# Performance work log

Hardware: AMD Instinct MI355X
Metric: run time of the kernel (lower is better)

The kernel has to match this reference:

```python
import jax, jax.numpy as jnp
import numpy as np

B, N, H = 16, 1024, 1024


def setup_inputs() -> dict:
    key = jax.random.key(0)
    ks = jax.random.split(key, 12)
    inv = 1.0 / np.sqrt(H)
    inp = {
        "x": jax.random.normal(ks[0], (B, N, H), jnp.float32),
        "atom_graph": jax.random.normal(ks[1], (B, N, N), jnp.float32),
        "variable_graph": jax.random.normal(ks[2], (B, N, N), jnp.float32),
        "Wq": jax.random.uniform(ks[3], (H, H), jnp.float32, -inv, inv),
        "bq": jax.random.uniform(ks[4], (H,), jnp.float32, -inv, inv),
        "Wk": jax.random.uniform(ks[5], (H, H), jnp.float32, -inv, inv),
        "bk": jax.random.uniform(ks[6], (H,), jnp.float32, -inv, inv),
        "Wv": jax.random.uniform(ks[7], (H, H), jnp.float32, -inv, inv),
        "bv": jax.random.uniform(ks[8], (H,), jnp.float32, -inv, inv),
        "predicate_pos": jax.random.randint(ks[9], (B, N), 0, 2, jnp.int32),
        "variable_tags": jax.random.randint(ks[10], (B, N), 0, 4, jnp.int32),
    }
    return inp


def _path_pool(h, predicate_pos):
    # h: [B,N,H]; predicate_pos: [B,N] in {0,1}
    b, n, d = h.shape
    i = jnp.arange(n)
    # pos[i-2] (value irrelevant for i<2, those branches handled explicitly)
    pp2 = jnp.pad(predicate_pos, ((0, 0), (2, 0)))[:, :n]  # [B,N]
    # window [s, e): i==0 -> [0,2); i==1 -> [0,3); pos[i-2]==1 -> [i,i+2); else [i-1,i+2)
    s = jnp.where(i < 2, 0, jnp.where(pp2 == 1, i, i - 1))  # [B,N]
    e = jnp.where(i == 0, 2, jnp.where(i == 1, 3, i + 2))    # [N]
    e = jnp.minimum(e, n)
    e = jnp.broadcast_to(e, (b, n))
    # prefix sums along node dim with a leading zero row -> windowed means via gather
    cs = jnp.concatenate([jnp.zeros((b, 1, d), h.dtype), jnp.cumsum(h, axis=1)], axis=1)  # [B,N+1,H]
    win_sum = (jnp.take_along_axis(cs, e[:, :, None], axis=1)
               - jnp.take_along_axis(cs, s[:, :, None], axis=1))  # [B,N,H]
    means = win_sum / (e - s)[:, :, None].astype(h.dtype)
    mask = (predicate_pos == 1).astype(h.dtype)  # [B,N]
    item = (means * mask[:, :, None]).sum(axis=1) / mask.sum(axis=1)[:, None]  # [B,H]
    return jnp.broadcast_to(item[:, None, :], (b, n, d))


def reference(x, atom_graph, variable_graph, Wq, bq, Wk, bk, Wv, bv,
              predicate_pos, variable_tags):
    scale = x.shape[-1] ** (-0.5)
    q = (x @ Wq.T + bq) * scale
    k = x @ Wk.T + bk
    v = x @ Wv.T + bv
    att = jnp.einsum("bnh,bmh->bnm", q, k) + atom_graph + variable_graph
    att = jax.nn.softmax(att, axis=-1)  # dropout is identity in eval
    h = jnp.einsum("bnm,bmh->bnh", att, v)
    return _path_pool(h, predicate_pos)
```

## Files before the change

kernel.cpp:

```cpp
#include <hip/hip_runtime.h>
#include <hip/hip_bf16.h>

#define BATCH 16
#define SEQ   1024
#define DIM   1024

typedef __attribute__((ext_vector_type(8))) short bf16x8;
typedef __attribute__((ext_vector_type(4))) float f32x4;
typedef __attribute__((ext_vector_type(4))) unsigned short us4;

__device__ __forceinline__ float bfu2f(unsigned short u) {
  union { unsigned int i; float f; } c; c.i = ((unsigned int)u) << 16; return c.f;
}
__device__ __forceinline__ unsigned short f2bfu(float f) {
  union { float f; unsigned int i; } c; c.f = f;
  return (unsigned short)((c.i + 0x7FFFu + ((c.i >> 16) & 1u)) >> 16);
}
__device__ __forceinline__ void async16(void* lds, const void* g) {
  __builtin_amdgcn_global_load_lds(
      (const __attribute__((address_space(1))) unsigned int*)g,
      (__attribute__((address_space(3))) unsigned int*)lds, 16, 0, 0);
}

__global__ void castT_kernel(const float* __restrict__ Wq, const float* __restrict__ Wk,
                             unsigned short* __restrict__ WqT,
                             unsigned short* __restrict__ WkT) {
  const float* in = (blockIdx.z == 0) ? Wq : Wk;
  unsigned short* out = (blockIdx.z == 0) ? WqT : WkT;
  __shared__ float t[64][65];
  const int h0 = blockIdx.x * 64, i0 = blockIdx.y * 64;
  const int tid = threadIdx.x;
  const int sub = tid >> 4, c4 = tid & 15;
#pragma unroll
  for (int p = 0; p < 4; ++p) {
    const int row = p * 16 + sub;
    f32x4 v = *(const f32x4*)(in + (size_t)(h0 + row) * DIM + i0 + c4 * 4);
    t[row][c4 * 4 + 0] = v[0]; t[row][c4 * 4 + 1] = v[1];
    t[row][c4 * 4 + 2] = v[2]; t[row][c4 * 4 + 3] = v[3];
  }
  __syncthreads();
#pragma unroll
  for (int p = 0; p < 4; ++p) {
    const int orow = p * 16 + sub;
    us4 o;
    o[0] = f2bfu(t[c4 * 4 + 0][orow]);
    o[1] = f2bfu(t[c4 * 4 + 1][orow]);
    o[2] = f2bfu(t[c4 * 4 + 2][orow]);
    o[3] = f2bfu(t[c4 * 4 + 3][orow]);
    *(us4*)(out + (size_t)(i0 + orow) * DIM + h0 + c4 * 4) = o;
  }
}

__global__ void t12_kernel(const unsigned short* __restrict__ WqT,
                           const unsigned short* __restrict__ WkT,
                           const float* __restrict__ bq, const float* __restrict__ bk,
                           float* __restrict__ t1, float* __restrict__ t2) {
  const int y = blockIdx.y;
  const unsigned short* Wt = y ? WkT : WqT;
  const float* vec = y ? bq : bk;
  float* tout = y ? t2 : t1;
  const int wave = threadIdx.x >> 6, lane = threadIdx.x & 63;
  const int i = blockIdx.x * 4 + wave;
  const us4* wr = (const us4*)(Wt + (size_t)i * DIM);
  float s = 0.f;
#pragma unroll
  for (int t = 0; t < 4; ++t) {
    us4 w4 = wr[lane + 64 * t];
    f32x4 b4 = *(const f32x4*)(vec + (lane + 64 * t) * 4);
    s += bfu2f(w4[0]) * b4[0] + bfu2f(w4[1]) * b4[1] +
         bfu2f(w4[2]) * b4[2] + bfu2f(w4[3]) * b4[3];
  }
#pragma unroll
  for (int o = 32; o; o >>= 1) s += __shfl_down(s, o);
  if (lane == 0) tout[i] = s;
}

__global__ void pathw_kernel(const int* __restrict__ pos,
                             const float* __restrict__ bq, const float* __restrict__ bk,
                             float* __restrict__ w, float* __restrict__ zbias,
                             float* __restrict__ dval) {
  const int b = blockIdx.x;
  __shared__ int ps[SEQ];
  __shared__ int mcnt;
  __shared__ float dred[4];
  const int tid = threadIdx.x;
  if (tid == 0) mcnt = 0;
  __syncthreads();
  if (b == 0) {
    for (int i = tid; i < DIM; i += 256) zbias[i] = 0.f;
    float dp = 0.f;
    for (int i = tid; i < DIM; i += 256) dp += bq[i] * bk[i];
#pragma unroll
    for (int o = 32; o; o >>= 1) dp += __shfl_down(dp, o);
    if ((tid & 63) == 0) dred[tid >> 6] = dp;
  }
  for (int i = tid; i < SEQ; i += 256) ps[i] = pos[b * SEQ + i];
  __syncthreads();
  if (b == 0 && tid == 0) dval[0] = dred[0] + dred[1] + dred[2] + dred[3];
  int c = 0;
  for (int i = tid; i < SEQ; i += 256) c += ps[i];
  for (int o = 32; o; o >>= 1) c += __shfl_down(c, o);
  if ((tid & 63) == 0) atomicAdd(&mcnt, c);
  __syncthreads();
  const float invM = 1.0f / (float)mcnt;
  for (int j = tid; j < SEQ; j += 256) {
    float a = 0.f;
#pragma unroll
    for (int di = -1; di <= 1; ++di) {
      int i = j + di;
      if (i < 0 || i >= SEQ) continue;
      if (!ps[i]) continue;
      int s, e;
      if (i < 2) { s = 0; e = (i == 0) ? 2 : 3; }
      else { s = (ps[i - 2] == 1) ? i : (i - 1); e = i + 2; if (e > SEQ) e = SEQ; }
      if (s <= j && j < e) a += 1.0f / (float)(e - s);
    }
    w[b * SEQ + j] = a * invM;
  }
}

__global__ void cast_row_kernel(const float* __restrict__ x, const float* __restrict__ Wv,
                                const float* __restrict__ t1, const float* __restrict__ t2,
                                const float* __restrict__ dval,
                                unsigned short* __restrict__ xb,
                                unsigned short* __restrict__ Wvb,
                                float* __restrict__ av, float* __restrict__ cvv) {
  const int blk = blockIdx.x;
  const int tid = threadIdx.x;
  if (blk >= BATCH * SEQ) {
    const int row = blk - BATCH * SEQ;
    const size_t base = (size_t)row * DIM + tid * 4;
    f32x4 v = *(const f32x4*)(Wv + base);
    us4 o;
    o[0] = f2bfu(v[0]); o[1] = f2bfu(v[1]); o[2] = f2bfu(v[2]); o[3] = f2bfu(v[3]);
    *(us4*)(Wvb + base) = o;
    return;
  }
  const size_t base = (size_t)blk * DIM + tid * 4;
  f32x4 v = *(const f32x4*)(x + base);
  us4 o;
  o[0] = f2bfu(v[0]); o[1] = f2bfu(v[1]); o[2] = f2bfu(v[2]); o[3] = f2bfu(v[3]);
  *(us4*)(xb + base) = o;
  const f32x4 q1 = *(const f32x4*)(t1 + tid * 4);
  const f32x4 q2 = *(const f32x4*)(t2 + tid * 4);
  float sa = v[0] * q1[0] + v[1] * q1[1] + v[2] * q1[2] + v[3] * q1[3];
  float sc = v[0] * q2[0] + v[1] * q2[1] + v[2] * q2[2] + v[3] * q2[3];
#pragma unroll
  for (int off = 32; off; off >>= 1) {
    sa += __shfl_down(sa, off);
    sc += __shfl_down(sc, off);
  }
  __shared__ float r1[4], r2[4];
  const int wave = tid >> 6, lane = tid & 63;
  if (lane == 0) { r1[wave] = sa; r2[wave] = sc; }
  __syncthreads();
  if (tid == 0) {
    const float scale = 0.03125f;
    av[blk]  = scale * (r1[0] + r1[1] + r1[2] + r1[3] + dval[0]);
    cvv[blk] = scale * (r2[0] + r2[1] + r2[2] + r2[3]);
  }
}

__global__ void proj_gemm(const unsigned short* __restrict__ A,
                          const unsigned short* __restrict__ W,
                          const float* __restrict__ bias, float alpha,
                          unsigned short* __restrict__ C, int M, int N, int K)
{
  __shared__ __align__(16) char smem[32768];
  float* Sl = (float*)smem;
  const int tid = threadIdx.x;
  const int wave = tid >> 6, lane = tid & 63;
  const int lr = lane & 15, lg = lane >> 4;
  const int wr = wave >> 1, wc = wave & 1;
  const int m0 = blockIdx.x * 128, n0 = blockIdx.y * 128;
  const int off0 = tid * 16, off1 = 4096 + tid * 16;
  const int r0 = off0 >> 6, ke0 = (off0 >> 1) & 31;
  const int r1 = off1 >> 6, ke1 = (off1 >> 1) & 31;
  f32x4 acc[4][4] = {};

  auto stage = [&](char* base, int kk) {
    async16(base + off0, A + (size_t)(m0 + r0) * K + kk + ke0);
    async16(base + off1, A + (size_t)(m0 + r1) * K + kk + ke1);
    async16(base + 8192 + off0, W + (size_t)(n0 + r0) * K + kk + ke0);
    async16(base + 8192 + off1, W + (size_t)(n0 + r1) * K + kk + ke1);
  };
  auto compute = [&](const char* base) {
    bf16x8 af[4], bfv[4];
#pragma unroll
    for (int i = 0; i < 4; ++i) {
      af[i]  = *(const bf16x8*)(base + ((wr * 64 + i * 16 + lr) << 6) + (lg << 4));
      bfv[i] = *(const bf16x8*)(base + 8192 + ((wc * 64 + i * 16 + lr) << 6) + (lg << 4));
    }
#pragma unroll
    for (int i = 0; i < 4; ++i)
#pragma unroll
      for (int j = 0; j < 4; ++j)
        acc[i][j] = __builtin_amdgcn_mfma_f32_16x16x32_bf16(af[i], bfv[j], acc[i][j], 0, 0, 0);
  };

  const int nt = K >> 5;
  stage(smem, 0);
  __syncthreads();
  int cur = 0;
  for (int k = 0; k < nt - 1; ++k) {
    stage(smem + ((cur ^ 1) << 14), (k + 1) << 5);
    compute(smem + (cur << 14));
    __syncthreads();
    cur ^= 1;
  }
  compute(smem + (cur << 14));
#pragma unroll
  for (int p = 0; p < 4; ++p) {
    __syncthreads();
    if (wr == (p >> 1)) {
      const int ibase = (p & 1) * 2;
#pragma unroll
      for (int ii = 0; ii < 2; ++ii) {
        const int i = ibase + ii;
#pragma unroll
        for (int j = 0; j < 4; ++j)
#pragma unroll
          for (int r = 0; r < 4; ++r)
            Sl[(ii * 16 + lg * 4 + r) * 132 + wc * 64 + j * 16 + lr] = acc[i][j][r];
      }
    }
    __syncthreads();
#pragma unroll
    for (int it = 0; it < 4; ++it) {
      const int v = tid + it * 256;
      const int lrow = v >> 5, c4 = v & 31;
      const int grow = m0 + p * 32 + lrow;
      const int col = n0 + c4 * 4;
      const f32x4 s4 = *(const f32x4*)(&Sl[lrow * 132 + c4 * 4]);
      const f32x4 b4 = *(const f32x4*)(bias + col);
      us4 o;
      o[0] = f2bfu((s4[0] + b4[0]) * alpha);
      o[1] = f2bfu((s4[1] + b4[1]) * alpha);
      o[2] = f2bfu((s4[2] + b4[2]) * alpha);
      o[3] = f2bfu((s4[3] + b4[3]) * alpha);
      *(us4*)(C + (size_t)grow * N + col) = o;
    }
  }
}

__global__ __launch_bounds__(512, 2)
void gemm256(const unsigned short* __restrict__ A,
             const unsigned short* __restrict__ B,
             unsigned short* __restrict__ C)
{
  extern __shared__ __align__(16) char smem[];
  const int gx = gridDim.x, gy = gridDim.y;
  const int flat = blockIdx.x + gx * (blockIdx.y + gy * blockIdx.z);
  const int q8 = (gx * gy * gridDim.z) >> 3;
  const int tt = (flat & 7) * q8 + (flat >> 3);
  const int bz = tt / (gx * gy);
  const int rem = tt - bz * (gx * gy);
  const int m0 = (rem / gx) * 256;
  const int n0 = (rem % gx) * 256;
  const size_t boff = (size_t)bz << 20;
  const int tid = threadIdx.x;
  const int lane = tid & 63;
  const int wid = tid >> 6;
  const int wm = wid >> 2, wn = wid & 3;
  const int lr = lane & 15, lg = lane >> 4;
  const unsigned short* Ab = A + boff;
  const unsigned short* Bb = B + boff;

  int sr[2], se[2], sL[2];
#pragma unroll
  for (int l = 0; l < 2; ++l) {
    const int L = l * 8192 + tid * 16;
    const int r = L >> 6, sp = (L >> 4) & 3;
    sL[l] = L; sr[l] = r; se[l] = (sp ^ ((r >> 1) & 3)) * 8;
  }
  int aoff[8], boff_[4];
#pragma unroll
  for (int i = 0; i < 8; ++i) {
    const int row = wm * 128 + i * 16 + lr;
    aoff[i] = row * 64 + (lg ^ ((row >> 1) & 3)) * 16;
  }
#pragma unroll
  for (int j = 0; j < 4; ++j) {
    const int row = wn * 64 + j * 16 + lr;
    boff_[j] = row * 64 + (lg ^ ((row >> 1) & 3)) * 16;
  }

  auto stage = [&](int slot, int kt) {
    char* sa = smem + slot * 32768;
#pragma unroll
    for (int l = 0; l < 2; ++l)
      async16(sa + sL[l], Ab + (size_t)(m0 + sr[l]) * DIM + kt * 32 + se[l]);
    char* sb = sa + 16384;
#pragma unroll
    for (int l = 0; l < 2; ++l)
      async16(sb + sL[l], Bb + (size_t)(n0 + sr[l]) * DIM + kt * 32 + se[l]);
  };

  f32x4 acc[8][4] = {};
  stage(0, 0); stage(1, 1); stage(2, 2); stage(3, 3);

#pragma unroll
  for (int t = 0; t < 32; ++t) {
    if (t == 0)       asm volatile("s_waitcnt vmcnt(12)" ::: "memory");
    else if (t <= 29) asm volatile("s_waitcnt vmcnt(8)" ::: "memory");
    else if (t == 30) asm volatile("s_waitcnt vmcnt(4)" ::: "memory");
    else              asm volatile("s_waitcnt vmcnt(0)" ::: "memory");
    __builtin_amdgcn_s_barrier();
    const char* sa = smem + (t & 3) * 32768;
    const char* sb = sa + 16384;
    bf16x8 a[8], bfr[4];
#pragma unroll
    for (int i = 0; i < 8; ++i) a[i] = *(const bf16x8*)(sa + aoff[i]);
#pragma unroll
    for (int j = 0; j < 4; ++j) bfr[j] = *(const bf16x8*)(sb + boff_[j]);
    if (t >= 1 && t <= 28) stage((t + 3) & 3, t + 3);
    __builtin_amdgcn_s_setprio(1);
#pragma unroll
    for (int i = 0; i < 8; ++i)
#pragma unroll
      for (int j = 0; j < 4; ++j)
        acc[i][j] = __builtin_amdgcn_mfma_f32_16x16x32_bf16(a[i], bfr[j], acc[i][j], 0, 0, 0);
    __builtin_amdgcn_s_setprio(0);
  }

  unsigned short* Sl = (unsigned short*)smem;
  unsigned short* Cb = C + boff;
#pragma unroll
  for (int half = 0; half < 2; ++half) {
    __syncthreads();
    if (wm == half) {
#pragma unroll
      for (int i = 0; i < 8; ++i)
#pragma unroll
        for (int j = 0; j < 4; ++j)
#pragma unroll
          for (int r = 0; r < 4; ++r)
            Sl[(i * 16 + lg * 4 + r) * 260 + wn * 64 + j * 16 + lr] =
                f2bfu(acc[i][j][r]);
    }
    __syncthreads();
#pragma unroll
    for (int it = 0; it < 16; ++it) {
      const int v = tid + it * 512;
      const int row = v >> 6, c4 = v & 63;
      *(us4*)(Cb + (size_t)(m0 + half * 128 + row) * SEQ + n0 + c4 * 4) =
          *(const us4*)(&Sl[row * 260 + c4 * 4]);
    }
  }
}

__global__ void exp_fused_kernel(const unsigned short* __restrict__ S,
                                 const float* __restrict__ ag, const float* __restrict__ vg,
                                 const float* __restrict__ av, const float* __restrict__ cv,
                                 const float* __restrict__ w, float* __restrict__ part)
{
  __shared__ float red[4][SEQ];
  const int b = blockIdx.y;
  const int tid = threadIdx.x;
  const int wave = tid >> 6, lane = tid & 63;
  const float* agb = ag + ((size_t)b << 20);
  const float* vgb = vg + ((size_t)b << 20);
  const unsigned short* Sb = S + ((size_t)b << 20);
  const float* cvb = cv + b * SEQ;
  f32x4 cq[4];
#pragma unroll
  for (int qi = 0; qi < 4; ++qi)
    cq[qi] = *(const f32x4*)(cvb + (lane + 64 * qi) * 4);
  f32x4 ur[4] = {};
  const int r0 = blockIdx.x * 8 + wave * 2;
  const float w0 = w[b * SEQ + r0];
  const float w1 = w[b * SEQ + r0 + 1];
  us4 sv[2][4]; f32x4 a4[2][4], g4[2][4];
#pragma unroll
  for (int r = 0; r < 2; ++r) {
    const float wr_ = r ? w1 : w0;
    if (wr_ == 0.f) continue;
    const int row = r0 + r;
#pragma unroll
    for (int qi = 0; qi < 4; ++qi) {
      const size_t base = (size_t)row * SEQ + (lane + 64 * qi) * 4;
      sv[r][qi] = *(const us4*)(Sb + base);
      a4[r][qi] = *(const f32x4*)(agb + base);
      g4[r][qi] = *(const f32x4*)(vgb + base);
    }
  }
#pragma unroll
  for (int r = 0; r < 2; ++r) {
    const float wr_ = r ? w1 : w0;
    if (wr_ == 0.f) continue;
    const int row = r0 + r;
    const float arow = av[b * SEQ + row];
    float e[16];
    float rs = 0.f;
#pragma unroll
    for (int qi = 0; qi < 4; ++qi)
#pragma unroll
      for (int j = 0; j < 4; ++j) {
        const float ev = __expf(bfu2f(sv[r][qi][j]) + a4[r][qi][j] + g4[r][qi][j] +
                                arow + cq[qi][j]);
        e[qi * 4 + j] = ev;
        rs += ev;
      }
#pragma unroll
    for (int o2 = 32; o2; o2 >>= 1) rs += __shfl_xor(rs, o2);
    const float cn = wr_ / rs;
#pragma unroll
    for (int qi = 0; qi < 4; ++qi)
#pragma unroll
      for (int j = 0; j < 4; ++j)
        ur[qi][j] += cn * e[qi * 4 + j];
  }
#pragma unroll
  for (int qi = 0; qi < 4; ++qi)
    *(f32x4*)(&red[wave][(lane + 64 * qi) * 4]) = ur[qi];
  __syncthreads();
  const int col = tid * 4;
  f32x4 s0 = *(const f32x4*)(&red[0][col]);
  const f32x4 s1 = *(const f32x4*)(&red[1][col]);
  const f32x4 s2 = *(const f32x4*)(&red[2][col]);
  const f32x4 s3 = *(const f32x4*)(&red[3][col]);
  s0[0] += s1[0] + s2[0] + s3[0];
  s0[1] += s1[1] + s2[1] + s3[1];
  s0[2] += s1[2] + s2[2] + s3[2];
  s0[3] += s1[3] + s2[3] + s3[3];
  *(f32x4*)(part + ((size_t)(b * 128 + blockIdx.x) << 10) + col) = s0;
}

__global__ void wcol_kernel(const unsigned short* __restrict__ Mt,
                            const float* __restrict__ wv,
                            const float* __restrict__ pin,
                            float* __restrict__ part) {
  const int nc = blockIdx.x;
  const int b = blockIdx.y;
  const int tid = threadIdx.x;
  __shared__ float c[64];
  if (pin) {
    const int n = nc * 64 + (tid & 63);
    const int bl0 = (tid >> 6) * 32;
    float s = 0.f;
#pragma unroll 8
    for (int bl = 0; bl < 32; ++bl)
      s += pin[((size_t)(b * 128 + bl0 + bl) << 10) + n];
    __shared__ float cp[4][64];
    cp[tid >> 6][tid & 63] = s;
    __syncthreads();
    if (tid < 64) c[tid] = cp[0][tid] + cp[1][tid] + cp[2][tid] + cp[3][tid];
  } else {
    if (tid < 64) c[tid] = wv[b * SEQ + nc * 64 + tid];
  }
  __syncthreads();
  const unsigned short* p = Mt + ((size_t)b << 20) + ((size_t)(nc * 64) << 10) + tid * 4;
  f32x4 acc = {0.f, 0.f, 0.f, 0.f};
#pragma unroll 8
  for (int n = 0; n < 64; ++n) {
    const us4 v = *(const us4*)(p + ((size_t)n << 10));
    const float cn = c[n];
    acc[0] += cn * bfu2f(v[0]); acc[1] += cn * bfu2f(v[1]);
    acc[2] += cn * bfu2f(v[2]); acc[3] += cn * bfu2f(v[3]);
  }
  *(f32x4*)(part + (size_t)((b * 16 + nc) << 10) + tid * 4) = acc;
}

__global__ void wred_kernel(const float* __restrict__ part, float* __restrict__ vec,
                            int nchunks) {
  const int b = blockIdx.x;
  const int tid = threadIdx.x;
  f32x4 s = {0.f, 0.f, 0.f, 0.f};
  for (int nc = 0; nc < nchunks; ++nc) {
    const f32x4 v = *(const f32x4*)(part + ((size_t)(b * nchunks + nc) << 10) + tid * 4);
    s[0] += v[0]; s[1] += v[1]; s[2] += v[2]; s[3] += v[3];
  }
  *(f32x4*)(vec + b * SEQ + tid * 4) = s;
}

__global__ void item_kernel(const float* __restrict__ y,
                            const unsigned short* __restrict__ Wvb,
                            const float* __restrict__ bv, float* __restrict__ item) {
  const int b = blockIdx.x;
  const int hblk = blockIdx.y;
  __shared__ float ys[DIM];
  const int tid = threadIdx.x;
  for (int i = tid; i < DIM; i += 256) ys[i] = y[b * DIM + i];
  __syncthreads();
  const int wave = tid >> 6, lane = tid & 63;
  const int h = hblk * 4 + wave;
  const us4* wrow = (const us4*)(Wvb + (size_t)h * DIM);
  float acc = 0.f;
#pragma unroll
  for (int t = 0; t < 4; ++t) {
    us4 v = wrow[t * 64 + lane];
    const int d0 = (t * 64 + lane) * 4;
    acc += ys[d0] * bfu2f(v[0]) + ys[d0 + 1] * bfu2f(v[1]) +
           ys[d0 + 2] * bfu2f(v[2]) + ys[d0 + 3] * bfu2f(v[3]);
  }
  for (int o = 32; o; o >>= 1) acc += __shfl_down(acc, o);
  if (lane == 0) item[b * DIM + h] = acc + bv[h];
}

__global__ void bcast_kernel(const float* __restrict__ item, float* __restrict__ out) {
  const int b = blockIdx.y;
  const int n = blockIdx.x;
  const f32x4* src = (const f32x4*)(item + b * DIM);
  f32x4* dst = (f32x4*)(out + (((size_t)b * SEQ + n) << 10));
  dst[threadIdx.x] = src[threadIdx.x];
}

extern "C" void kernel_launch(void* const* d_in, const int* in_sizes, int n_in,
                              void* d_out, int out_size, void* d_ws, size_t ws_size,
                              hipStream_t stream) {
  const float* x    = (const float*)d_in[0];
  const float* ag   = (const float*)d_in[1];
  const float* vgr  = (const float*)d_in[2];
  const float* Wq   = (const float*)d_in[3];
  const float* bq   = (const float*)d_in[4];
  const float* Wk   = (const float*)d_in[5];
  const float* bk   = (const float*)d_in[6];
  const float* Wv   = (const float*)d_in[7];
  const float* bv   = (const float*)d_in[8];
  const int*   pos  = (const int*)d_in[9];
  float* out = (float*)d_out;

  char* ws = (char*)d_ws;
  size_t off = 0;
  auto alloc = [&](size_t bytes) { void* p = ws + off; off += (bytes + 255) & ~(size_t)255; return p; };
  const size_t BNH = (size_t)BATCH * SEQ * DIM;
  unsigned short* xb   = (unsigned short*)alloc(BNH * 2);
  unsigned short* zb   = (unsigned short*)alloc(BNH * 2);
  unsigned short* S    = (unsigned short*)alloc(BNH * 2);
  unsigned short* WqT  = (unsigned short*)alloc((size_t)DIM * DIM * 2);
  unsigned short* WkT  = (unsigned short*)alloc((size_t)DIM * DIM * 2);
  unsigned short* Wvb  = (unsigned short*)alloc((size_t)DIM * DIM * 2);
  unsigned short* Hb   = (unsigned short*)alloc((size_t)DIM * DIM * 2);
  float* w     = (float*)alloc((size_t)BATCH * SEQ * 4);
  float* av    = (float*)alloc((size_t)BATCH * SEQ * 4);
  float* cvv   = (float*)alloc((size_t)BATCH * SEQ * 4);
  float* t1    = (float*)alloc((size_t)DIM * 4);
  float* t2    = (float*)alloc((size_t)DIM * 4);
  float* zbias = (float*)alloc((size_t)DIM * 4);
  float* dval  = (float*)alloc(256);
  float* y     = (float*)alloc((size_t)BATCH * DIM * 4);
  float* item  = (float*)alloc((size_t)BATCH * DIM * 4);
  float* partU = (float*)alloc((size_t)BATCH * 128 * SEQ * 4);
  float* partY = (float*)alloc((size_t)BATCH * 16 * SEQ * 4);

  const float scale = 0.03125f;

  (void)hipFuncSetAttribute(reinterpret_cast<const void*>(gemm256),
                            hipFuncAttributeMaxDynamicSharedMemorySize, 131072);

  castT_kernel<<<dim3(16, 16, 2), 256, 0, stream>>>(Wq, Wk, WqT, WkT);
  t12_kernel<<<dim3(256, 2), 256, 0, stream>>>(WqT, WkT, bq, bk, t1, t2);
  pathw_kernel<<<BATCH, 256, 0, stream>>>(pos, bq, bk, w, zbias, dval);

  cast_row_kernel<<<BATCH * SEQ + DIM, 256, 0, stream>>>(x, Wv, t1, t2, dval,
                                                         xb, Wvb, av, cvv);

  proj_gemm<<<dim3(8, 8), 256, 0, stream>>>(WkT, WqT, zbias, scale, Hb, DIM, DIM, DIM);

  gemm256<<<dim3(4, 64, 1), 512, 131072, stream>>>(xb, Hb, zb);

  gemm256<<<dim3(4, 4, BATCH), 512, 131072, stream>>>(zb, xb, S);

  exp_fused_kernel<<<dim3(128, BATCH), 256, 0, stream>>>(S, ag, vgr, av, cvv, w, partU);

  wcol_kernel<<<dim3(16, BATCH), 256, 0, stream>>>(xb, nullptr, partU, partY);
  wred_kernel<<<BATCH, 256, 0, stream>>>(partY, y, 16);

  item_kernel<<<dim3(BATCH, 256), 256, 0, stream>>>(y, Wvb, bv, item);

  bcast_kernel<<<dim3(SEQ, BATCH), 256, 0, stream>>>(item, out);
}
```

Measured before the change: 192.7 us.

## Fuse softmax exponent and row denominators into the score GEMM epilogue

The exponent step (adding atom/variable graph biases, then exp) moves into the epilogue of the batched score GEMM. The epilogue writes unnormalised bf16 exponentials and accumulates per-row denominators with atomics. The per-row weights are then normalised in the column-weighting pass, so the separate exp kernel and its large partial-sum buffer go away. In exchange there is an extra wcol/wred pass over the exponential matrix, and memory-bound epilogue work now runs inside a GEMM launched at one block per CU. Rows with zero weight are never written but are still read, so leftover NaN contents in the workspace could leak into the result.

```diff
diff --git a/kernel.cpp b/kernel.cpp
--- a/kernel.cpp
+++ b/kernel.cpp
@@ -77,8 +77,8 @@
 
 __global__ void pathw_kernel(const int* __restrict__ pos,
                              const float* __restrict__ bq, const float* __restrict__ bk,
-                             float* __restrict__ w, float* __restrict__ zbias,
-                             float* __restrict__ dval) {
+                             float* __restrict__ w, float* __restrict__ denom,
+                             float* __restrict__ zbias, float* __restrict__ dval) {
   const int b = blockIdx.x;
   __shared__ int ps[SEQ];
   __shared__ int mcnt;
@@ -94,7 +94,10 @@
     for (int o = 32; o; o >>= 1) dp += __shfl_down(dp, o);
     if ((tid & 63) == 0) dred[tid >> 6] = dp;
   }
-  for (int i = tid; i < SEQ; i += 256) ps[i] = pos[b * SEQ + i];
+  for (int i = tid; i < SEQ; i += 256) {
+    ps[i] = pos[b * SEQ + i];
+    denom[b * SEQ + i] = 0.f;
+  }
   __syncthreads();
   if (b == 0 && tid == 0) dval[0] = dred[0] + dred[1] + dred[2] + dred[3];
   int c = 0;
@@ -349,104 +352,153 @@
   }
 }
 
-__global__ void exp_fused_kernel(const unsigned short* __restrict__ S,
-                                 const float* __restrict__ ag, const float* __restrict__ vg,
-                                 const float* __restrict__ av, const float* __restrict__ cv,
-                                 const float* __restrict__ w, float* __restrict__ part)
+__global__ __launch_bounds__(512, 1)
+void gemm256exp(const unsigned short* __restrict__ A,
+                const unsigned short* __restrict__ B,
+                const float* __restrict__ ag, const float* __restrict__ vg,
+                const float* __restrict__ av, const float* __restrict__ cv,
+                const float* __restrict__ w,
+                unsigned short* __restrict__ E, float* __restrict__ denom)
 {
-  __shared__ float red[4][SEQ];
-  const int b = blockIdx.y;
-  const int tid = threadIdx.x;
-  const int wave = tid >> 6, lane = tid & 63;
-  const float* agb = ag + ((size_t)b << 20);
-  const float* vgb = vg + ((size_t)b << 20);
-  const unsigned short* Sb = S + ((size_t)b << 20);
-  const float* cvb = cv + b * SEQ;
-  f32x4 cq[4];
-#pragma unroll
-  for (int qi = 0; qi < 4; ++qi)
-    cq[qi] = *(const f32x4*)(cvb + (lane + 64 * qi) * 4);
-  f32x4 ur[4] = {};
-  const int r0 = blockIdx.x * 8 + wave * 2;
-  const float w0 = w[b * SEQ + r0];
-  const float w1 = w[b * SEQ + r0 + 1];
-  us4 sv[2][4]; f32x4 a4[2][4], g4[2][4];
-#pragma unroll
-  for (int r = 0; r < 2; ++r) {
-    const float wr_ = r ? w1 : w0;
-    if (wr_ == 0.f) continue;
-    const int row = r0 + r;
-#pragma unroll
-    for (int qi = 0; qi < 4; ++qi) {
-      const size_t base = (size_t)row * SEQ + (lane + 64 * qi) * 4;
-      sv[r][qi] = *(const us4*)(Sb + base);
-      a4[r][qi] = *(const f32x4*)(agb + base);
-      g4[r][qi] = *(const f32x4*)(vgb + base);
-    }
-  }
-#pragma unroll
-  for (int r = 0; r < 2; ++r) {
-    const float wr_ = r ? w1 : w0;
-    if (wr_ == 0.f) continue;
-    const int row = r0 + r;
-    const float arow = av[b * SEQ + row];
-    float e[16];
-    float rs = 0.f;
-#pragma unroll
-    for (int qi = 0; qi < 4; ++qi)
-#pragma unroll
-      for (int j = 0; j < 4; ++j) {
-        const float ev = __expf(bfu2f(sv[r][qi][j]) + a4[r][qi][j] + g4[r][qi][j] +
-                                arow + cq[qi][j]);
-        e[qi * 4 + j] = ev;
-        rs += ev;
-      }
-#pragma unroll
-    for (int o2 = 32; o2; o2 >>= 1) rs += __shfl_xor(rs, o2);
-    const float cn = wr_ / rs;
-#pragma unroll
-    for (int qi = 0; qi < 4; ++qi)
+  extern __shared__ __align__(16) char smem[];
+  const int gx = gridDim.x, gy = gridDim.y;
+  const int flat = blockIdx.x + gx * (blockIdx.y + gy * blockIdx.z);
+  const int q8 = (gx * gy * gridDim.z) >> 3;
+  const int tt = (flat & 7) * q8 + (flat >> 3);
+  const int bz = tt / (gx * gy);
+  const int rem = tt - bz * (gx * gy);
+  const int m0 = (rem / gx) * 256;
+  const int n0 = (rem % gx) * 256;
+  const size_t boff = (size_t)bz << 20;
+  const int tid = threadIdx.x;
+  const int lane = tid & 63;
+  const int wid = tid >> 6;
+  const int wm = wid >> 2, wn = wid & 3;
+  const int lr = lane & 15, lg = lane >> 4;
+  const unsigned short* Ab = A + boff;
+  const unsigned short* Bb = B + boff;
+
+  int sr[2], se[2], sL[2];
+#pragma unroll
+  for (int l = 0; l < 2; ++l) {
+    const int L = l * 8192 + tid * 16;
+    const int r = L >> 6, sp = (L >> 4) & 3;
+    sL[l] = L; sr[l] = r; se[l] = (sp ^ ((r >> 1) & 3)) * 8;
+  }
+  int aoff[8], boff_[4];
+#pragma unroll
+  for (int i = 0; i < 8; ++i) {
+    const int row = wm * 128 + i * 16 + lr;
+    aoff[i] = row * 64 + (lg ^ ((row >> 1) & 3)) * 16;
+  }
+#pragma unroll
+  for (int j = 0; j < 4; ++j) {
+    const int row = wn * 64 + j * 16 + lr;
+    boff_[j] = row * 64 + (lg ^ ((row >> 1) & 3)) * 16;
+  }
+
+  auto stage = [&](int slot, int kt) {
+    char* sa = smem + slot * 32768;
+#pragma unroll
+    for (int l = 0; l < 2; ++l)
+      async16(sa + sL[l], Ab + (size_t)(m0 + sr[l]) * DIM + kt * 32 + se[l]);
+    char* sb = sa + 16384;
+#pragma unroll
+    for (int l = 0; l < 2; ++l)
+      async16(sb + sL[l], Bb + (size_t)(n0 + sr[l]) * DIM + kt * 32 + se[l]);
+  };
+
+  f32x4 acc[8][4] = {};
+  stage(0, 0); stage(1, 1); stage(2, 2); stage(3, 3);
+
+#pragma unroll
+  for (int t = 0; t < 32; ++t) {
+    if (t == 0)       asm volatile("s_waitcnt vmcnt(12)" ::: "memory");
+    else if (t <= 29) asm volatile("s_waitcnt vmcnt(8)" ::: "memory");
+    else if (t == 30) asm volatile("s_waitcnt vmcnt(4)" ::: "memory");
+    else              asm volatile("s_waitcnt vmcnt(0)" ::: "memory");
+    __builtin_amdgcn_s_barrier();
+    const char* sa = smem + (t & 3) * 32768;
+    const char* sb = sa + 16384;
+    bf16x8 a[8], bfr[4];
+#pragma unroll
+    for (int i = 0; i < 8; ++i) a[i] = *(const bf16x8*)(sa + aoff[i]);
+#pragma unroll
+    for (int j = 0; j < 4; ++j) bfr[j] = *(const bf16x8*)(sb + boff_[j]);
+    if (t >= 1 && t <= 28) stage((t + 3) & 3, t + 3);
+    __builtin_amdgcn_s_setprio(1);
+#pragma unroll
+    for (int i = 0; i < 8; ++i)
 #pragma unroll
       for (int j = 0; j < 4; ++j)
-        ur[qi][j] += cn * e[qi * 4 + j];
-  }
-#pragma unroll
-  for (int qi = 0; qi < 4; ++qi)
-    *(f32x4*)(&red[wave][(lane + 64 * qi) * 4]) = ur[qi];
-  __syncthreads();
-  const int col = tid * 4;
-  f32x4 s0 = *(const f32x4*)(&red[0][col]);
-  const f32x4 s1 = *(const f32x4*)(&red[1][col]);
-  const f32x4 s2 = *(const f32x4*)(&red[2][col]);
-  const f32x4 s3 = *(const f32x4*)(&red[3][col]);
-  s0[0] += s1[0] + s2[0] + s3[0];
-  s0[1] += s1[1] + s2[1] + s3[1];
-  s0[2] += s1[2] + s2[2] + s3[2];
-  s0[3] += s1[3] + s2[3] + s3[3];
-  *(f32x4*)(part + ((size_t)(b * 128 + blockIdx.x) << 10) + col) = s0;
+        acc[i][j] = __builtin_amdgcn_mfma_f32_16x16x32_bf16(a[i], bfr[j], acc[i][j], 0, 0, 0);
+    __builtin_amdgcn_s_setprio(0);
+  }
+
+  unsigned short* Sl = (unsigned short*)smem;
+  unsigned short* Eb = E + boff;
+  const float* agb = ag + boff;
+  const float* vgb = vg + boff;
+  const float* cvb = cv + (size_t)bz * SEQ;
+  const float* avb = av + (size_t)bz * SEQ;
+  const float* wb  = w  + (size_t)bz * SEQ;
+  float* dnb = denom + (size_t)bz * SEQ;
+#pragma unroll
+  for (int half = 0; half < 2; ++half) {
+    __syncthreads();
+    if (wm == half) {
+#pragma unroll
+      for (int i = 0; i < 8; ++i)
+#pragma unroll
+        for (int j = 0; j < 4; ++j)
+#pragma unroll
+          for (int r = 0; r < 4; ++r)
+            Sl[(i * 16 + lg * 4 + r) * 260 + wn * 64 + j * 16 + lr] =
+                f2bfu(acc[i][j][r]);
+    }
+    __syncthreads();
+#pragma unroll
+    for (int it = 0; it < 16; ++it) {
+      const int row = it * 8 + wid;
+      const int grow = m0 + half * 128 + row;
+      const float wrow = wb[grow];
+      if (wrow == 0.f) continue;
+      const int col = n0 + lane * 4;
+      const size_t base = (size_t)grow * SEQ + col;
+      const us4 sv = *(const us4*)(&Sl[row * 260 + lane * 4]);
+      const f32x4 a4 = *(const f32x4*)(agb + base);
+      const f32x4 g4 = *(const f32x4*)(vgb + base);
+      const f32x4 c4 = *(const f32x4*)(cvb + col);
+      const float arow = avb[grow];
+      const float e0 = __expf(bfu2f(sv[0]) + a4[0] + g4[0] + arow + c4[0]);
+      const float e1 = __expf(bfu2f(sv[1]) + a4[1] + g4[1] + arow + c4[1]);
+      const float e2 = __expf(bfu2f(sv[2]) + a4[2] + g4[2] + arow + c4[2]);
+      const float e3 = __expf(bfu2f(sv[3]) + a4[3] + g4[3] + arow + c4[3]);
+      us4 o;
+      o[0] = f2bfu(e0); o[1] = f2bfu(e1); o[2] = f2bfu(e2); o[3] = f2bfu(e3);
+      *(us4*)(Eb + base) = o;
+      float rs = e0 + e1 + e2 + e3;
+#pragma unroll
+      for (int o2 = 32; o2; o2 >>= 1) rs += __shfl_down(rs, o2);
+      if (lane == 0) atomicAdd(&dnb[grow], rs);
+    }
+  }
 }
 
 __global__ void wcol_kernel(const unsigned short* __restrict__ Mt,
                             const float* __restrict__ wv,
-                            const float* __restrict__ pin,
+                            const float* __restrict__ dv,
                             float* __restrict__ part) {
   const int nc = blockIdx.x;
   const int b = blockIdx.y;
   const int tid = threadIdx.x;
   __shared__ float c[64];
-  if (pin) {
-    const int n = nc * 64 + (tid & 63);
-    const int bl0 = (tid >> 6) * 32;
-    float s = 0.f;
-#pragma unroll 8
-    for (int bl = 0; bl < 32; ++bl)
-      s += pin[((size_t)(b * 128 + bl0 + bl) << 10) + n];
-    __shared__ float cp[4][64];
-    cp[tid >> 6][tid & 63] = s;
-    __syncthreads();
-    if (tid < 64) c[tid] = cp[0][tid] + cp[1][tid] + cp[2][tid] + cp[3][tid];
-  } else {
-    if (tid < 64) c[tid] = wv[b * SEQ + nc * 64 + tid];
+  if (tid < 64) {
+    const int n = nc * 64 + tid;
+    const float wn = wv[b * SEQ + n];
+    float cvw = wn;
+    if (dv) cvw = (wn == 0.f) ? 0.f : wn / dv[b * SEQ + n];
+    c[tid] = cvw;
   }
   __syncthreads();
   const unsigned short* p = Mt + ((size_t)b << 20) + ((size_t)(nc * 64) << 10) + tid * 4;
@@ -526,12 +578,14 @@
   const size_t BNH = (size_t)BATCH * SEQ * DIM;
   unsigned short* xb   = (unsigned short*)alloc(BNH * 2);
   unsigned short* zb   = (unsigned short*)alloc(BNH * 2);
-  unsigned short* S    = (unsigned short*)alloc(BNH * 2);
+  unsigned short* E    = (unsigned short*)alloc(BNH * 2);
   unsigned short* WqT  = (unsigned short*)alloc((size_t)DIM * DIM * 2);
   unsigned short* WkT  = (unsigned short*)alloc((size_t)DIM * DIM * 2);
   unsigned short* Wvb  = (unsigned short*)alloc((size_t)DIM * DIM * 2);
   unsigned short* Hb   = (unsigned short*)alloc((size_t)DIM * DIM * 2);
   float* w     = (float*)alloc((size_t)BATCH * SEQ * 4);
+  float* denom = (float*)alloc((size_t)BATCH * SEQ * 4);
+  float* u     = (float*)alloc((size_t)BATCH * SEQ * 4);
   float* av    = (float*)alloc((size_t)BATCH * SEQ * 4);
   float* cvv   = (float*)alloc((size_t)BATCH * SEQ * 4);
   float* t1    = (float*)alloc((size_t)DIM * 4);
@@ -540,17 +594,18 @@
   float* dval  = (float*)alloc(256);
   float* y     = (float*)alloc((size_t)BATCH * DIM * 4);
   float* item  = (float*)alloc((size_t)BATCH * DIM * 4);
-  float* partU = (float*)alloc((size_t)BATCH * 128 * SEQ * 4);
   float* partY = (float*)alloc((size_t)BATCH * 16 * SEQ * 4);
 
   const float scale = 0.03125f;
 
   (void)hipFuncSetAttribute(reinterpret_cast<const void*>(gemm256),
                             hipFuncAttributeMaxDynamicSharedMemorySize, 131072);
+  (void)hipFuncSetAttribute(reinterpret_cast<const void*>(gemm256exp),
+                            hipFuncAttributeMaxDynamicSharedMemorySize, 131072);
 
   castT_kernel<<<dim3(16, 16, 2), 256, 0, stream>>>(Wq, Wk, WqT, WkT);
   t12_kernel<<<dim3(256, 2), 256, 0, stream>>>(WqT, WkT, bq, bk, t1, t2);
-  pathw_kernel<<<BATCH, 256, 0, stream>>>(pos, bq, bk, w, zbias, dval);
+  pathw_kernel<<<BATCH, 256, 0, stream>>>(pos, bq, bk, w, denom, zbias, dval);
 
   cast_row_kernel<<<BATCH * SEQ + DIM, 256, 0, stream>>>(x, Wv, t1, t2, dval,
                                                          xb, Wvb, av, cvv);
@@ -559,11 +614,13 @@
 
   gemm256<<<dim3(4, 64, 1), 512, 131072, stream>>>(xb, Hb, zb);
 
-  gemm256<<<dim3(4, 4, BATCH), 512, 131072, stream>>>(zb, xb, S);
-
-  exp_fused_kernel<<<dim3(128, BATCH), 256, 0, stream>>>(S, ag, vgr, av, cvv, w, partU);
-
-  wcol_kernel<<<dim3(16, BATCH), 256, 0, stream>>>(xb, nullptr, partU, partY);
+  gemm256exp<<<dim3(4, 4, BATCH), 512, 131072, stream>>>(zb, xb, ag, vgr, av, cvv,
+                                                         w, E, denom);
+
+  wcol_kernel<<<dim3(16, BATCH), 256, 0, stream>>>(E, w, denom, partY);
+  wred_kernel<<<BATCH, 256, 0, stream>>>(partY, u, 16);
+
+  wcol_kernel<<<dim3(16, BATCH), 256, 0, stream>>>(xb, u, nullptr, partY);
   wred_kernel<<<BATCH, 256, 0, stream>>>(partY, y, 16);
 
   item_kernel<<<dim3(BATCH, 256), 256, 0, stream>>>(y, Wvb, bv, item);
```

Measured after the change: 217.1 us. +12.7%, slower.
